# Optimization experiments

Measured on AMD Instinct MI355X. Metric: run time of the kernel, lower is better.

## Reference

```python
import jax, jax.numpy as jnp
import numpy as np

N_NODES = 50000
D_FEAT = 512
N_EDGES = 100000


def setup_inputs() -> dict:
    key = jax.random.key(0)
    k0, k1, k2, k3, k4 = jax.random.split(key, 5)
    return {
        "out": jax.random.normal(k0, (N_NODES, D_FEAT), dtype=jnp.float32),
        "pos_src": jax.random.randint(k1, (N_EDGES,), 0, N_NODES),
        "pos_dst": jax.random.randint(k2, (N_EDGES,), 0, N_NODES),
        "neg_src": jax.random.randint(k3, (N_EDGES,), 0, N_NODES),
        "neg_dst": jax.random.randint(k4, (N_EDGES,), 0, N_NODES),
    }


def _edge_scores(out, src, dst):
    # per-edge u . v dot product (fn.u_dot_v): gather + reduce over feature dim
    return jnp.sum(out[src] * out[dst], axis=-1)  # [E]


def reference(out, pos_src, pos_dst, neg_src, neg_dst):
    pos_score = _edge_scores(out, pos_src, pos_dst)  # [E_pos]
    neg_score = _edge_scores(out, neg_src, neg_dst)  # [E_neg]
    score = jnp.concatenate([pos_score, neg_score])  # [E_pos + E_neg]
    label = jnp.concatenate([
        jnp.ones(pos_score.shape[0], dtype=score.dtype),
        jnp.zeros(neg_score.shape[0], dtype=score.dtype),
    ])
    # numerically-stable binary_cross_entropy_with_logits, mean reduction
    loss = jnp.mean(
        jnp.maximum(score, 0.0) - score * label + jnp.log1p(jnp.exp(-jnp.abs(score)))
    )
    return loss
```

## Files before the change

### kernel.cpp

```cpp
#include <hip/hip_runtime.h>
#include <math.h>

#define D_FEAT 512
#define WAVES_PER_BLOCK 4
#define NBLOCKS 2048

typedef unsigned int uint32;

__device__ __forceinline__ float bf_lo(uint32 w) { return __uint_as_float(w << 16); }
__device__ __forceinline__ float bf_hi(uint32 w) { return __uint_as_float(w & 0xffff0000u); }

__global__ __launch_bounds__(256) void convert_bf16(
    const float* __restrict__ feat, uint32* __restrict__ bt, int n8)
{
    const float4* f4 = (const float4*)feat;
    const int stride = gridDim.x * blockDim.x;
    for (int i = blockIdx.x * blockDim.x + threadIdx.x; i < n8; i += stride) {
        float4 a = f4[2*i], b = f4[2*i + 1];
        const float src[8] = {a.x, a.y, a.z, a.w, b.x, b.y, b.z, b.w};
        uint32 w[8];
        #pragma unroll
        for (int k = 0; k < 8; ++k) {
            uint32 u = __float_as_uint(src[k]);
            u = u + 0x7fffu + ((u >> 16) & 1u);
            w[k] = u >> 16;
        }
        uint4 o;
        o.x = w[0] | (w[1] << 16);
        o.y = w[2] | (w[3] << 16);
        o.z = w[4] | (w[5] << 16);
        o.w = w[6] | (w[7] << 16);
        ((uint4*)bt)[i] = o;
    }
}

__global__ __launch_bounds__(256) void edge_bce_bf16(
    const uint32* __restrict__ bt,
    const int* __restrict__ pos_src, const int* __restrict__ pos_dst,
    const int* __restrict__ neg_src, const int* __restrict__ neg_dst,
    int n_edges, double* __restrict__ partials)
{
    const int lane = threadIdx.x & 63;
    const int sub  = lane & 31;
    const int half = lane >> 5;
    const int wave = threadIdx.x >> 6;
    const int slot = (blockIdx.x * WAVES_PER_BLOCK + wave) * 2 + half;
    const int n_slots = gridDim.x * WAVES_PER_BLOCK * 2;
    const int total = 2 * n_edges;

    double acc = 0.0;
    for (int e = slot; e < total; e += n_slots) {
        const bool pos = e < n_edges;
        const int  i   = pos ? e : e - n_edges;
        const int  src = pos ? pos_src[i] : neg_src[i];
        const int  dst = pos ? pos_dst[i] : neg_dst[i];
        const uint4* u = (const uint4*)(bt + (size_t)src * (D_FEAT / 2));
        const uint4* v = (const uint4*)(bt + (size_t)dst * (D_FEAT / 2));
        uint4 u0 = u[sub], u1 = u[sub + 32];
        uint4 v0 = v[sub], v1 = v[sub + 32];

        float d =
              bf_lo(u0.x)*bf_lo(v0.x) + bf_hi(u0.x)*bf_hi(v0.x)
            + bf_lo(u0.y)*bf_lo(v0.y) + bf_hi(u0.y)*bf_hi(v0.y)
            + bf_lo(u0.z)*bf_lo(v0.z) + bf_hi(u0.z)*bf_hi(v0.z)
            + bf_lo(u0.w)*bf_lo(v0.w) + bf_hi(u0.w)*bf_hi(v0.w)
            + bf_lo(u1.x)*bf_lo(v1.x) + bf_hi(u1.x)*bf_hi(v1.x)
            + bf_lo(u1.y)*bf_lo(v1.y) + bf_hi(u1.y)*bf_hi(v1.y)
            + bf_lo(u1.z)*bf_lo(v1.z) + bf_hi(u1.z)*bf_hi(v1.z)
            + bf_lo(u1.w)*bf_lo(v1.w) + bf_hi(u1.w)*bf_hi(v1.w);

        #pragma unroll
        for (int off = 1; off <= 16; off <<= 1) d += __shfl_xor(d, off, 64);

        if (sub == 0) {
            float s = d;
            float t = fmaxf(s, 0.0f) - (pos ? s : 0.0f) + log1pf(expf(-fabsf(s)));
            acc += (double)t;
        }
    }

    __shared__ double wsum[WAVES_PER_BLOCK * 2];
    if (sub == 0) wsum[wave * 2 + half] = acc;
    __syncthreads();
    if (threadIdx.x == 0) {
        double b = 0.0;
        #pragma unroll
        for (int i = 0; i < WAVES_PER_BLOCK * 2; ++i) b += wsum[i];
        partials[blockIdx.x] = b;
    }
}

__global__ __launch_bounds__(256) void edge_bce_partial(
    const float* __restrict__ feat,
    const int* __restrict__ pos_src, const int* __restrict__ pos_dst,
    const int* __restrict__ neg_src, const int* __restrict__ neg_dst,
    int n_edges, double* __restrict__ partials)
{
    const int lane = threadIdx.x & 63;
    const int wave = threadIdx.x >> 6;
    const int wave_global = blockIdx.x * WAVES_PER_BLOCK + wave;
    const int n_waves = gridDim.x * WAVES_PER_BLOCK;
    const int total = 2 * n_edges;

    double acc = 0.0;
    for (int e = wave_global; e < total; e += n_waves) {
        int src, dst; float label;
        if (e < n_edges) { src = pos_src[e]; dst = pos_dst[e]; label = 1.0f; }
        else { src = neg_src[e - n_edges]; dst = neg_dst[e - n_edges]; label = 0.0f; }
        const float4* u = (const float4*)(feat + (size_t)src * D_FEAT);
        const float4* v = (const float4*)(feat + (size_t)dst * D_FEAT);
        float4 u0 = u[lane], u1 = u[lane + 64];
        float4 v0 = v[lane], v1 = v[lane + 64];
        float d = u0.x*v0.x + u0.y*v0.y + u0.z*v0.z + u0.w*v0.w
                + u1.x*v1.x + u1.y*v1.y + u1.z*v1.z + u1.w*v1.w;
        #pragma unroll
        for (int off = 32; off; off >>= 1) d += __shfl_xor(d, off, 64);
        if (lane == 0) {
            float s = d;
            acc += (double)(fmaxf(s, 0.0f) - s * label + log1pf(expf(-fabsf(s))));
        }
    }
    __shared__ double wsum[WAVES_PER_BLOCK];
    if (lane == 0) wsum[wave] = acc;
    __syncthreads();
    if (threadIdx.x == 0) {
        double b = 0.0;
        #pragma unroll
        for (int i = 0; i < WAVES_PER_BLOCK; ++i) b += wsum[i];
        partials[blockIdx.x] = b;
    }
}

__global__ __launch_bounds__(256) void reduce_partials(
    const double* __restrict__ partials, int n, float* __restrict__ out_scalar,
    double inv_count)
{
    double a = 0.0;
    for (int i = threadIdx.x; i < n; i += 256) a += partials[i];
    #pragma unroll
    for (int off = 32; off; off >>= 1) a += __shfl_xor(a, off, 64);
    __shared__ double w[4];
    const int lane = threadIdx.x & 63, wv = threadIdx.x >> 6;
    if (lane == 0) w[wv] = a;
    __syncthreads();
    if (threadIdx.x == 0) {
        out_scalar[0] = (float)((w[0] + w[1] + w[2] + w[3]) * inv_count);
    }
}

extern "C" void kernel_launch(void* const* d_in, const int* in_sizes, int n_in,
                              void* d_out, int out_size, void* d_ws, size_t ws_size,
                              hipStream_t stream) {
    const float* feat    = (const float*)d_in[0];
    const int*   pos_src = (const int*)d_in[1];
    const int*   pos_dst = (const int*)d_in[2];
    const int*   neg_src = (const int*)d_in[3];
    const int*   neg_dst = (const int*)d_in[4];
    const int n_edges = in_sizes[1];
    const int n_feat  = in_sizes[0];

    double* partials = (double*)d_ws;
    float*  out      = (float*)d_out;

    const size_t bt_off   = (size_t)NBLOCKS * sizeof(double);
    const size_t bt_bytes = (size_t)n_feat * 2;
    const bool   use_bf16 = ws_size >= bt_off + bt_bytes;

    if (use_bf16) {
        uint32* bt = (uint32*)((char*)d_ws + bt_off);
        convert_bf16<<<NBLOCKS, 256, 0, stream>>>(feat, bt, n_feat / 8);
        edge_bce_bf16<<<NBLOCKS, 256, 0, stream>>>(
            bt, pos_src, pos_dst, neg_src, neg_dst, n_edges, partials);
    } else {
        edge_bce_partial<<<NBLOCKS, 256, 0, stream>>>(
            feat, pos_src, pos_dst, neg_src, neg_dst, n_edges, partials);
    }
    reduce_partials<<<1, 256, 0, stream>>>(
        partials, NBLOCKS, out, 1.0 / (2.0 * (double)n_edges));
}
```

Before: 220.8 us.

## Switch gathered features from bf16 to fp16 with fdot2 and two-edge unroll

Converts node features to fp16 instead of bf16 and computes the per-edge dot products with the packed fdot2 instruction, which cuts the ALU work for unpacking and multiplying. The edge loop is also unrolled to handle two edges per half-wave at once, so more independent gathers are in flight to hide memory latency. fp16 has less range than bf16, so large feature values could overflow, and the extra registers may lower occupancy.

```diff
diff --git a/kernel.cpp b/kernel.cpp
--- a/kernel.cpp
+++ b/kernel.cpp
@@ -6,36 +6,60 @@
 #define NBLOCKS 2048
 
 typedef unsigned int uint32;
-
-__device__ __forceinline__ float bf_lo(uint32 w) { return __uint_as_float(w << 16); }
-__device__ __forceinline__ float bf_hi(uint32 w) { return __uint_as_float(w & 0xffff0000u); }
-
-__global__ __launch_bounds__(256) void convert_bf16(
-    const float* __restrict__ feat, uint32* __restrict__ bt, int n8)
+typedef _Float16 half2v __attribute__((ext_vector_type(2)));
+
+__global__ __launch_bounds__(256) void convert_f16(
+    const float* __restrict__ feat, uint32* __restrict__ ht, int n8)
 {
     const float4* f4 = (const float4*)feat;
     const int stride = gridDim.x * blockDim.x;
     for (int i = blockIdx.x * blockDim.x + threadIdx.x; i < n8; i += stride) {
         float4 a = f4[2*i], b = f4[2*i + 1];
-        const float src[8] = {a.x, a.y, a.z, a.w, b.x, b.y, b.z, b.w};
+        const float s[8] = {a.x, a.y, a.z, a.w, b.x, b.y, b.z, b.w};
+        uint4 o;
         uint32 w[8];
         #pragma unroll
         for (int k = 0; k < 8; ++k) {
-            uint32 u = __float_as_uint(src[k]);
-            u = u + 0x7fffu + ((u >> 16) & 1u);
-            w[k] = u >> 16;
-        }
-        uint4 o;
+            half2v h; h.x = (_Float16)s[k]; h.y = (_Float16)0.f;
+            w[k] = (uint32)__builtin_bit_cast(uint32, h) & 0xffffu;
+        }
         o.x = w[0] | (w[1] << 16);
         o.y = w[2] | (w[3] << 16);
         o.z = w[4] | (w[5] << 16);
         o.w = w[6] | (w[7] << 16);
-        ((uint4*)bt)[i] = o;
-    }
-}
-
-__global__ __launch_bounds__(256) void edge_bce_bf16(
-    const uint32* __restrict__ bt,
+        ((uint4*)ht)[i] = o;
+    }
+}
+
+__device__ __forceinline__ float dot_u4(uint4 a, uint4 b, float acc) {
+#if __has_builtin(__builtin_amdgcn_fdot2)
+    acc = __builtin_amdgcn_fdot2(__builtin_bit_cast(half2v, a.x),
+                                 __builtin_bit_cast(half2v, b.x), acc, false);
+    acc = __builtin_amdgcn_fdot2(__builtin_bit_cast(half2v, a.y),
+                                 __builtin_bit_cast(half2v, b.y), acc, false);
+    acc = __builtin_amdgcn_fdot2(__builtin_bit_cast(half2v, a.z),
+                                 __builtin_bit_cast(half2v, b.z), acc, false);
+    acc = __builtin_amdgcn_fdot2(__builtin_bit_cast(half2v, a.w),
+                                 __builtin_bit_cast(half2v, b.w), acc, false);
+#else
+    const uint32 aw[4] = {a.x, a.y, a.z, a.w};
+    const uint32 bw[4] = {b.x, b.y, b.z, b.w};
+    #pragma unroll
+    for (int k = 0; k < 4; ++k) {
+        half2v ah = __builtin_bit_cast(half2v, aw[k]);
+        half2v bh = __builtin_bit_cast(half2v, bw[k]);
+        acc += (float)ah.x * (float)bh.x + (float)ah.y * (float)bh.y;
+    }
+#endif
+    return acc;
+}
+
+__device__ __forceinline__ float bce_term(float s, bool pos) {
+    return fmaxf(s, 0.0f) - (pos ? s : 0.0f) + log1pf(expf(-fabsf(s)));
+}
+
+__global__ __launch_bounds__(256) void edge_bce_f16(
+    const uint32* __restrict__ ht,
     const int* __restrict__ pos_src, const int* __restrict__ pos_dst,
     const int* __restrict__ neg_src, const int* __restrict__ neg_dst,
     int n_edges, double* __restrict__ partials)
@@ -49,34 +73,54 @@
     const int total = 2 * n_edges;
 
     double acc = 0.0;
-    for (int e = slot; e < total; e += n_slots) {
+    int e = slot;
+
+    for (; e + n_slots < total; e += 2 * n_slots) {
+        const int eA = e, eB = e + n_slots;
+        const bool pA = eA < n_edges, pB = eB < n_edges;
+        const int iA = pA ? eA : eA - n_edges;
+        const int iB = pB ? eB : eB - n_edges;
+        const int srcA = pA ? pos_src[iA] : neg_src[iA];
+        const int dstA = pA ? pos_dst[iA] : neg_dst[iA];
+        const int srcB = pB ? pos_src[iB] : neg_src[iB];
+        const int dstB = pB ? pos_dst[iB] : neg_dst[iB];
+
+        const uint4* uA = (const uint4*)(ht + (size_t)srcA * (D_FEAT / 2));
+        const uint4* vA = (const uint4*)(ht + (size_t)dstA * (D_FEAT / 2));
+        const uint4* uB = (const uint4*)(ht + (size_t)srcB * (D_FEAT / 2));
+        const uint4* vB = (const uint4*)(ht + (size_t)dstB * (D_FEAT / 2));
+
+        uint4 a0 = uA[sub], a1 = uA[sub + 32];
+        uint4 b0 = vA[sub], b1 = vA[sub + 32];
+        uint4 c0 = uB[sub], c1 = uB[sub + 32];
+        uint4 d0 = vB[sub], d1 = vB[sub + 32];
+
+        float dA = dot_u4(a1, b1, dot_u4(a0, b0, 0.0f));
+        float dB = dot_u4(c1, d1, dot_u4(c0, d0, 0.0f));
+
+        #pragma unroll
+        for (int off = 1; off <= 16; off <<= 1) {
+            dA += __shfl_xor(dA, off, 64);
+            dB += __shfl_xor(dB, off, 64);
+        }
+        if (sub == 0) {
+            acc += (double)bce_term(dA, pA);
+            acc += (double)bce_term(dB, pB);
+        }
+    }
+    for (; e < total; e += n_slots) {
         const bool pos = e < n_edges;
         const int  i   = pos ? e : e - n_edges;
         const int  src = pos ? pos_src[i] : neg_src[i];
         const int  dst = pos ? pos_dst[i] : neg_dst[i];
-        const uint4* u = (const uint4*)(bt + (size_t)src * (D_FEAT / 2));
-        const uint4* v = (const uint4*)(bt + (size_t)dst * (D_FEAT / 2));
+        const uint4* u = (const uint4*)(ht + (size_t)src * (D_FEAT / 2));
+        const uint4* v = (const uint4*)(ht + (size_t)dst * (D_FEAT / 2));
         uint4 u0 = u[sub], u1 = u[sub + 32];
         uint4 v0 = v[sub], v1 = v[sub + 32];
-
-        float d =
-              bf_lo(u0.x)*bf_lo(v0.x) + bf_hi(u0.x)*bf_hi(v0.x)
-            + bf_lo(u0.y)*bf_lo(v0.y) + bf_hi(u0.y)*bf_hi(v0.y)
-            + bf_lo(u0.z)*bf_lo(v0.z) + bf_hi(u0.z)*bf_hi(v0.z)
-            + bf_lo(u0.w)*bf_lo(v0.w) + bf_hi(u0.w)*bf_hi(v0.w)
-            + bf_lo(u1.x)*bf_lo(v1.x) + bf_hi(u1.x)*bf_hi(v1.x)
-            + bf_lo(u1.y)*bf_lo(v1.y) + bf_hi(u1.y)*bf_hi(v1.y)
-            + bf_lo(u1.z)*bf_lo(v1.z) + bf_hi(u1.z)*bf_hi(v1.z)
-            + bf_lo(u1.w)*bf_lo(v1.w) + bf_hi(u1.w)*bf_hi(v1.w);
-
+        float d = dot_u4(u1, v1, dot_u4(u0, v0, 0.0f));
         #pragma unroll
         for (int off = 1; off <= 16; off <<= 1) d += __shfl_xor(d, off, 64);
-
-        if (sub == 0) {
-            float s = d;
-            float t = fmaxf(s, 0.0f) - (pos ? s : 0.0f) + log1pf(expf(-fabsf(s)));
-            acc += (double)t;
-        }
+        if (sub == 0) acc += (double)bce_term(d, pos);
     }
 
     __shared__ double wsum[WAVES_PER_BLOCK * 2];
@@ -162,15 +206,15 @@
     double* partials = (double*)d_ws;
     float*  out      = (float*)d_out;
 
-    const size_t bt_off   = (size_t)NBLOCKS * sizeof(double);
-    const size_t bt_bytes = (size_t)n_feat * 2;
-    const bool   use_bf16 = ws_size >= bt_off + bt_bytes;
-
-    if (use_bf16) {
-        uint32* bt = (uint32*)((char*)d_ws + bt_off);
-        convert_bf16<<<NBLOCKS, 256, 0, stream>>>(feat, bt, n_feat / 8);
-        edge_bce_bf16<<<NBLOCKS, 256, 0, stream>>>(
-            bt, pos_src, pos_dst, neg_src, neg_dst, n_edges, partials);
+    const size_t ht_off   = (size_t)NBLOCKS * sizeof(double);
+    const size_t ht_bytes = (size_t)n_feat * 2;
+    const bool   use_f16  = ws_size >= ht_off + ht_bytes;
+
+    if (use_f16) {
+        uint32* ht = (uint32*)((char*)d_ws + ht_off);
+        convert_f16<<<NBLOCKS, 256, 0, stream>>>(feat, ht, n_feat / 8);
+        edge_bce_f16<<<NBLOCKS, 256, 0, stream>>>(
+            ht, pos_src, pos_dst, neg_src, neg_dst, n_edges, partials);
     } else {
         edge_bce_partial<<<NBLOCKS, 256, 0, stream>>>(
             feat, pos_src, pos_dst, neg_src, neg_dst, n_edges, partials);
```

Result: no change. 222.2 us (+0.6%).
